# Kernel optimization log

Hardware: AMD Instinct MI355X
Metric: run time of the kernel (lower is better)

Reference implementation:

```python
import jax, jax.numpy as jnp
import numpy as np

N_NODES = 100000
N_EDGES = 1200000
D_IN = 64
D_HID = 64


def setup_inputs() -> dict:
    key = jax.random.key(0)
    k1, k2, k3, k4, k5 = jax.random.split(key, 5)
    src = jax.random.randint(k1, (N_EDGES,), 0, N_NODES, dtype=jnp.int32)
    dst = jax.random.randint(k2, (N_EDGES,), 0, N_NODES, dtype=jnp.int32)
    w = jax.random.uniform(k3, (N_EDGES,), dtype=jnp.float32)
    data = jax.random.normal(k4, (N_NODES, D_IN), dtype=jnp.float32)
    theta = jax.random.normal(k5, (D_IN, D_HID), dtype=jnp.float32)
    return {"src": src, "dst": dst, "w": w, "data": data, "theta": theta,
            "num_nodes": N_NODES}


def reference(src, dst, w, data, theta, num_nodes):
    # weighted gather of source-node features: [E, D_IN]
    weighted = w[:, None] * data[src]
    # scatter-add into destination nodes: [N, D_IN]
    agg = jax.ops.segment_sum(weighted, dst, num_segments=num_nodes)
    # dense projection: [N, D_HID]
    return jnp.dot(agg, theta)
```

## Files before the change

kernel.cpp:

```cpp
#include <hip/hip_runtime.h>

#define D 64
#define NPB 128
#define NPB_SHIFT 7
#define MAXB 1024
#define SCATTER_T 512
#define CHUNK_MAX 4704
#define CAPB 2560
#define GT 512

__device__ inline unsigned f2bf(float f) {
    unsigned u = __float_as_uint(f);
    return (u + 0x7FFFu + ((u >> 16) & 1u)) >> 16;
}

__global__ void zero_i_kernel(int* __restrict__ p, int n) {
    int i = blockIdx.x * blockDim.x + threadIdx.x;
    if (i < n) p[i] = 0;
}
__global__ void zero_f4_kernel(float4* __restrict__ p, int n4) {
    int i = blockIdx.x * blockDim.x + threadIdx.x;
    if (i < n4) p[i] = make_float4(0.f, 0.f, 0.f, 0.f);
}

__global__ __launch_bounds__(SCATTER_T) void bucket_scatter_kernel(
        const int* __restrict__ src, const int* __restrict__ dst,
        const float* __restrict__ w, int* __restrict__ cursor,
        int* __restrict__ ovfCnt, int4* __restrict__ ovf,
        int2* __restrict__ adjB, int E, int B) {
    __shared__ int lc[MAXB];
    __shared__ int lpre[MAXB];
    __shared__ int lbase[MAXB];
    __shared__ int lfill[MAXB];
    __shared__ int sums[SCATTER_T];
    __shared__ unsigned short sb[CHUNK_MAX];
    __shared__ int2 stage[CHUNK_MAX];

    int t = threadIdx.x;
    int chunk = (E + gridDim.x - 1) / gridDim.x;
    int lo = blockIdx.x * chunk, hi = min(lo + chunk, E);
    int n = hi - lo;
    if (n <= 0) return;

    for (int i = t; i < MAXB; i += SCATTER_T) { lc[i] = 0; lfill[i] = 0; }
    __syncthreads();

    for (int e = lo + t; e < hi; e += SCATTER_T)
        atomicAdd(&lc[dst[e] >> NPB_SHIFT], 1);
    __syncthreads();

    int s0 = lc[2 * t], s1 = lc[2 * t + 1];
    sums[t] = s0 + s1;
    __syncthreads();
    for (int st = 1; st < SCATTER_T; st <<= 1) {
        int v = (t >= st) ? sums[t - st] : 0;
        __syncthreads();
        sums[t] += v;
        __syncthreads();
    }
    int ex = (t == 0) ? 0 : sums[t - 1];
    lpre[2 * t]     = ex;
    lpre[2 * t + 1] = ex + s0;
    __syncthreads();

    for (int i = t; i < B; i += SCATTER_T) {
        int c = lc[i];
        lbase[i] = c ? atomicAdd(&cursor[i], c) : 0;
    }
    __syncthreads();

    for (int e = lo + t; e < hi; e += SCATTER_T) {
        int d = dst[e];
        int bkt = d >> NPB_SHIFT;
        int i = lpre[bkt] + atomicAdd(&lfill[bkt], 1);
        stage[i] = make_int2(src[e] | ((d & (NPB - 1)) << 20), __float_as_int(w[e]));
        sb[i] = (unsigned short)bkt;
    }
    __syncthreads();

    for (int i = t; i < n; i += SCATTER_T) {
        int bkt = sb[i];
        int2 v = stage[i];
        int pos = lbase[bkt] + (i - lpre[bkt]);
        if (pos < CAPB) {
            adjB[(size_t)bkt * CAPB + pos] = v;
        } else {
            int oi = atomicAdd(ovfCnt, 1);
            ovf[oi] = make_int4(v.x, v.y, bkt, 0);
        }
    }
}

__global__ __launch_bounds__(GT) void sort_gather_kernel(
        const int2* __restrict__ adjB, const int* __restrict__ cursor,
        const int* __restrict__ ovfCnt, const int4* __restrict__ ovf,
        const unsigned* __restrict__ projU, float* __restrict__ out, int N) {
    __shared__ int cnt[NPB];
    __shared__ int pre[NPB];
    __shared__ int fill[NPB];
    __shared__ int2 ladj[CAPB];
    __shared__ int sOvf;

    int b = blockIdx.x;
    int t = threadIdx.x;
    int total = cursor[b];
    int m = min(total, CAPB);
    const int2* base = adjB + (size_t)b * CAPB;

    if (t < NPB) { cnt[t] = 0; fill[t] = 0; }
    if (t == 0) sOvf = *ovfCnt;
    __syncthreads();
    for (int e = t; e < m; e += GT)
        atomicAdd(&cnt[((unsigned)base[e].x) >> 20], 1);
    __syncthreads();
    if (t < NPB) pre[t] = cnt[t];
    __syncthreads();
    for (int st = 1; st < NPB; st <<= 1) {
        int v = (t < NPB && t >= st) ? pre[t - st] : 0;
        __syncthreads();
        if (t < NPB) pre[t] += v;
        __syncthreads();
    }
    for (int e = t; e < m; e += GT) {
        int2 a = base[e];
        int dL = ((unsigned)a.x) >> 20;
        int pos = ((dL == 0) ? 0 : pre[dL - 1]) + atomicAdd(&fill[dL], 1);
        ladj[pos] = make_int2(a.x & 0xFFFFF, a.y);
    }
    __syncthreads();

    int wave = t >> 6;
    int lane = t & 63;
    int half = lane >> 5;
    int k = lane & 31;

#pragma unroll 1
    for (int i = 0; i < NPB / 8; ++i) {
        int dL = wave * (NPB / 8) + i;
        int node = b * NPB + dL;
        if (node >= N) break;
        int rb = (dL == 0) ? 0 : pre[dL - 1];
        int re = pre[dL];
        float2 accA = make_float2(0.f, 0.f);
        float2 accB = make_float2(0.f, 0.f);
        int j = rb + half;
        for (; j + 2 < re; j += 4) {
            int2 a0 = ladj[j];
            int2 a1 = ladj[j + 2];
            float w0 = __int_as_float(a0.y);
            float w1 = __int_as_float(a1.y);
            unsigned p0 = projU[(size_t)a0.x * 32 + k];
            unsigned p1 = projU[(size_t)a1.x * 32 + k];
            accA.x += w0 * __uint_as_float(p0 << 16);
            accA.y += w0 * __uint_as_float(p0 & 0xFFFF0000u);
            accB.x += w1 * __uint_as_float(p1 << 16);
            accB.y += w1 * __uint_as_float(p1 & 0xFFFF0000u);
        }
        if (j < re) {
            int2 a0 = ladj[j];
            float w0 = __int_as_float(a0.y);
            unsigned p0 = projU[(size_t)a0.x * 32 + k];
            accA.x += w0 * __uint_as_float(p0 << 16);
            accA.y += w0 * __uint_as_float(p0 & 0xFFFF0000u);
        }
        float2 acc = make_float2(accA.x + accB.x, accA.y + accB.y);
        acc.x += __shfl(acc.x, lane ^ 32, 64);
        acc.y += __shfl(acc.y, lane ^ 32, 64);
        if (half == 0)
            *(float2*)&out[(size_t)node * D + 2 * k] = acc;
    }

    if (sOvf > 0) {
        __syncthreads();
        for (int e = t; e < sOvf; e += GT) {
            int4 o = ovf[e];
            if (o.z != b) continue;
            int dL = ((unsigned)o.x) >> 20;
            int node = b * NPB + dL;
            if (node >= N) continue;
            float wgt = __int_as_float(o.y);
            int s = o.x & 0xFFFFF;
            for (int d2 = 0; d2 < D / 2; ++d2) {
                unsigned p = projU[(size_t)s * 32 + d2];
                atomicAdd(&out[(size_t)node * D + 2 * d2],     wgt * __uint_as_float(p << 16));
                atomicAdd(&out[(size_t)node * D + 2 * d2 + 1], wgt * __uint_as_float(p & 0xFFFF0000u));
            }
        }
    }
}

__global__ __launch_bounds__(256, 4) void rowgemm_bf16_kernel(const float* __restrict__ A,
                                                              const float* __restrict__ theta,
                                                              unsigned short* __restrict__ proj16,
                                                              int N) {
    __shared__ float th[D * D];
    __shared__ float at[D][68];
    int t = threadIdx.x;
    int rowBase = blockIdx.x * 64;

#pragma unroll
    for (int i = 0; i < 4; ++i) {
        int f = t + i * 256;
        ((float4*)th)[f] = ((const float4*)theta)[f];
    }
#pragma unroll
    for (int i = 0; i < 4; ++i) {
        int f = t + i * 256;
        int row = f >> 4;
        int kv = f & 15;
        float4 v = make_float4(0.f, 0.f, 0.f, 0.f);
        if (rowBase + row < N) v = *(const float4*)&A[(size_t)(rowBase + row) * D + kv * 4];
        at[kv * 4 + 0][row] = v.x;
        at[kv * 4 + 1][row] = v.y;
        at[kv * 4 + 2][row] = v.z;
        at[kv * 4 + 3][row] = v.w;
    }
    __syncthreads();

    int c0 = (t & 15) * 4;
    int r0 = (t >> 4) * 4;
    float4 acc0 = make_float4(0.f, 0.f, 0.f, 0.f);
    float4 acc1 = acc0, acc2 = acc0, acc3 = acc0;

#pragma unroll 16
    for (int k = 0; k < D; ++k) {
        float4 bv = *(const float4*)&th[k * D + c0];
        float4 av = *(const float4*)&at[k][r0];
        acc0.x += av.x * bv.x; acc0.y += av.x * bv.y; acc0.z += av.x * bv.z; acc0.w += av.x * bv.w;
        acc1.x += av.y * bv.x; acc1.y += av.y * bv.y; acc1.z += av.y * bv.z; acc1.w += av.y * bv.w;
        acc2.x += av.z * bv.x; acc2.y += av.z * bv.y; acc2.z += av.z * bv.z; acc2.w += av.z * bv.w;
        acc3.x += av.w * bv.x; acc3.y += av.w * bv.y; acc3.z += av.w * bv.z; acc3.w += av.w * bv.w;
    }

    float4 accs[4] = {acc0, acc1, acc2, acc3};
#pragma unroll
    for (int i = 0; i < 4; ++i) {
        int r = rowBase + r0 + i;
        if (r < N) {
            unsigned lo = f2bf(accs[i].x) | (f2bf(accs[i].y) << 16);
            unsigned hi = f2bf(accs[i].z) | (f2bf(accs[i].w) << 16);
            *(uint2*)&proj16[(size_t)r * D + c0] = make_uint2(lo, hi);
        }
    }
}

__global__ void scatter_kernel(const int* __restrict__ src, const int* __restrict__ dst,
                               const float* __restrict__ w, const float* __restrict__ data,
                               float* __restrict__ agg, int E) {
    int tid = blockIdx.x * blockDim.x + threadIdx.x;
    int e = tid >> 6;
    int d = tid & 63;
    if (e >= E) return;
    float val = w[e] * data[(size_t)src[e] * D + d];
    atomicAdd(&agg[(size_t)dst[e] * D + d], val);
}

__global__ __launch_bounds__(256, 4) void rowgemm_f32_kernel(const float* __restrict__ A,
                                                             const float* __restrict__ theta,
                                                             float* __restrict__ out, int N) {
    __shared__ float th[D * D];
    __shared__ float at[D][68];
    int t = threadIdx.x;
    int rowBase = blockIdx.x * 64;
#pragma unroll
    for (int i = 0; i < 4; ++i) {
        int f = t + i * 256;
        ((float4*)th)[f] = ((const float4*)theta)[f];
    }
#pragma unroll
    for (int i = 0; i < 4; ++i) {
        int f = t + i * 256;
        int row = f >> 4;
        int kv = f & 15;
        float4 v = make_float4(0.f, 0.f, 0.f, 0.f);
        if (rowBase + row < N) v = *(const float4*)&A[(size_t)(rowBase + row) * D + kv * 4];
        at[kv * 4 + 0][row] = v.x;
        at[kv * 4 + 1][row] = v.y;
        at[kv * 4 + 2][row] = v.z;
        at[kv * 4 + 3][row] = v.w;
    }
    __syncthreads();
    int c0 = (t & 15) * 4;
    int r0 = (t >> 4) * 4;
    float4 acc0 = make_float4(0.f, 0.f, 0.f, 0.f);
    float4 acc1 = acc0, acc2 = acc0, acc3 = acc0;
#pragma unroll 16
    for (int kk = 0; kk < D; ++kk) {
        float4 bv = *(const float4*)&th[kk * D + c0];
        float4 av = *(const float4*)&at[kk][r0];
        acc0.x += av.x * bv.x; acc0.y += av.x * bv.y; acc0.z += av.x * bv.z; acc0.w += av.x * bv.w;
        acc1.x += av.y * bv.x; acc1.y += av.y * bv.y; acc1.z += av.y * bv.z; acc1.w += av.y * bv.w;
        acc2.x += av.z * bv.x; acc2.y += av.z * bv.y; acc2.z += av.z * bv.z; acc2.w += av.z * bv.w;
        acc3.x += av.w * bv.x; acc3.y += av.w * bv.y; acc3.z += av.w * bv.z; acc3.w += av.w * bv.w;
    }
    float4 accs[4] = {acc0, acc1, acc2, acc3};
#pragma unroll
    for (int i = 0; i < 4; ++i) {
        int r = rowBase + r0 + i;
        if (r < N) *(float4*)&out[(size_t)r * D + c0] = accs[i];
    }
}

extern "C" void kernel_launch(void* const* d_in, const int* in_sizes, int n_in,
                              void* d_out, int out_size, void* d_ws, size_t ws_size,
                              hipStream_t stream) {
    const int*   src   = (const int*)d_in[0];
    const int*   dst   = (const int*)d_in[1];
    const float* w     = (const float*)d_in[2];
    const float* data  = (const float*)d_in[3];
    const float* theta = (const float*)d_in[4];
    const int E = in_sizes[0];
    const int N = in_sizes[3] / D;
    float* out = (float*)d_out;

    const int B = (N + NPB - 1) / NPB;

    size_t projBytes = (size_t)N * D * 2;
    size_t adjBytes  = (size_t)B * CAPB * 8;
    size_t ovfBytes  = (size_t)E * 16;
    size_t need = projBytes + adjBytes + ovfBytes + ((size_t)B + 1) * 4 + 256;

    if (ws_size >= need && N < (1 << 20) && B <= MAXB) {
        unsigned short* proj16 = (unsigned short*)d_ws;
        int2* adjB   = (int2*)((char*)d_ws + projBytes);
        int4* ovf    = (int4*)((char*)d_ws + projBytes + adjBytes);
        int*  cursor = (int*)((char*)d_ws + projBytes + adjBytes + ovfBytes);
        int*  ovfCnt = cursor + B;

        int g = (E + CHUNK_MAX - 1) / CHUNK_MAX;

        zero_i_kernel<<<(B + 1 + 255) / 256, 256, 0, stream>>>(cursor, B + 1);
        bucket_scatter_kernel<<<g, SCATTER_T, 0, stream>>>(src, dst, w, cursor, ovfCnt, ovf, adjB, E, B);
        rowgemm_bf16_kernel<<<(N + 63) / 64, 256, 0, stream>>>(data, theta, proj16, N);
        sort_gather_kernel<<<B, GT, 0, stream>>>(adjB, cursor, ovfCnt, ovf, (const unsigned*)proj16, out, N);
    } else {
        float* agg = (float*)d_ws;
        int n4 = (N * D) / 4;
        zero_f4_kernel<<<(n4 + 255) / 256, 256, 0, stream>>>((float4*)agg, n4);
        long long total = (long long)E * D;
        scatter_kernel<<<(int)((total + 255) / 256), 256, 0, stream>>>(src, dst, w, data, agg, E);
        rowgemm_f32_kernel<<<(N + 63) / 64, 256, 0, stream>>>(agg, theta, out, N);
    }
}
```

Measured before the change: 163.9 us.

## Fuse bucket scatter and bf16 projection GEMM into one launch, register-prefetch edges

Merges the bucket-scatter and row-GEMM kernels into a single launch that branches on block index, sharing a union of shared memory, so both phases can run concurrently and one launch is removed. The scatter path loads each thread's edges into registers once instead of reading dst twice from global memory. The gather kernel also keeps adjacency entries in registers between its count and placement passes. Its per-node loop now gives each half-wave its own node with a 4-way unrolled edge loop, which drops the cross-half shuffle. The cost is more registers per thread, a larger shared footprint for GEMM blocks, and a scatter grid clamped to at least 256 blocks.

```diff
diff --git a/kernel.cpp b/kernel.cpp
--- a/kernel.cpp
+++ b/kernel.cpp
@@ -6,8 +6,10 @@
 #define MAXB 1024
 #define SCATTER_T 512
 #define CHUNK_MAX 4704
+#define SCQ 10
 #define CAPB 2560
 #define GT 512
+#define GQ 5
 
 __device__ inline unsigned f2bf(float f) {
     unsigned u = __float_as_uint(f);
@@ -23,70 +25,147 @@
     if (i < n4) p[i] = make_float4(0.f, 0.f, 0.f, 0.f);
 }
 
-__global__ __launch_bounds__(SCATTER_T) void bucket_scatter_kernel(
+union FusedSMem {
+    struct {
+        int lc[MAXB];
+        int lpre[MAXB];
+        int lbase[MAXB];
+        int lfill[MAXB];
+        int sums[SCATTER_T];
+        unsigned short sb[CHUNK_MAX];
+        int2 stage[CHUNK_MAX];
+    } sc;
+    struct {
+        float th[D * D];
+        float at[D][68];
+    } gm;
+};
+
+__global__ __launch_bounds__(SCATTER_T, 4) void fused_scatter_gemm_kernel(
         const int* __restrict__ src, const int* __restrict__ dst,
-        const float* __restrict__ w, int* __restrict__ cursor,
+        const float* __restrict__ w, const float* __restrict__ data,
+        const float* __restrict__ theta, int* __restrict__ cursor,
         int* __restrict__ ovfCnt, int4* __restrict__ ovf,
-        int2* __restrict__ adjB, int E, int B) {
-    __shared__ int lc[MAXB];
-    __shared__ int lpre[MAXB];
-    __shared__ int lbase[MAXB];
-    __shared__ int lfill[MAXB];
-    __shared__ int sums[SCATTER_T];
-    __shared__ unsigned short sb[CHUNK_MAX];
-    __shared__ int2 stage[CHUNK_MAX];
-
+        int2* __restrict__ adjB, unsigned short* __restrict__ proj16,
+        int E, int B, int N, int gs) {
+    __shared__ FusedSMem sm;
     int t = threadIdx.x;
-    int chunk = (E + gridDim.x - 1) / gridDim.x;
-    int lo = blockIdx.x * chunk, hi = min(lo + chunk, E);
-    int n = hi - lo;
-    if (n <= 0) return;
-
-    for (int i = t; i < MAXB; i += SCATTER_T) { lc[i] = 0; lfill[i] = 0; }
-    __syncthreads();
-
-    for (int e = lo + t; e < hi; e += SCATTER_T)
-        atomicAdd(&lc[dst[e] >> NPB_SHIFT], 1);
-    __syncthreads();
-
-    int s0 = lc[2 * t], s1 = lc[2 * t + 1];
-    sums[t] = s0 + s1;
-    __syncthreads();
-    for (int st = 1; st < SCATTER_T; st <<= 1) {
-        int v = (t >= st) ? sums[t - st] : 0;
-        __syncthreads();
-        sums[t] += v;
-        __syncthreads();
-    }
-    int ex = (t == 0) ? 0 : sums[t - 1];
-    lpre[2 * t]     = ex;
-    lpre[2 * t + 1] = ex + s0;
-    __syncthreads();
-
-    for (int i = t; i < B; i += SCATTER_T) {
-        int c = lc[i];
-        lbase[i] = c ? atomicAdd(&cursor[i], c) : 0;
-    }
-    __syncthreads();
-
-    for (int e = lo + t; e < hi; e += SCATTER_T) {
-        int d = dst[e];
-        int bkt = d >> NPB_SHIFT;
-        int i = lpre[bkt] + atomicAdd(&lfill[bkt], 1);
-        stage[i] = make_int2(src[e] | ((d & (NPB - 1)) << 20), __float_as_int(w[e]));
-        sb[i] = (unsigned short)bkt;
-    }
-    __syncthreads();
-
-    for (int i = t; i < n; i += SCATTER_T) {
-        int bkt = sb[i];
-        int2 v = stage[i];
-        int pos = lbase[bkt] + (i - lpre[bkt]);
-        if (pos < CAPB) {
-            adjB[(size_t)bkt * CAPB + pos] = v;
-        } else {
-            int oi = atomicAdd(ovfCnt, 1);
-            ovf[oi] = make_int4(v.x, v.y, bkt, 0);
+
+    if ((int)blockIdx.x < gs) {
+        int chunk = (E + gs - 1) / gs;
+        int lo = blockIdx.x * chunk, hi = min(lo + chunk, E);
+        if (hi - lo <= 0) return;
+        int n = hi - lo;
+
+        for (int i = t; i < MAXB; i += SCATTER_T) { sm.sc.lc[i] = 0; sm.sc.lfill[i] = 0; }
+
+        int rd[SCQ]; int rs[SCQ]; float rw[SCQ];
+#pragma unroll
+        for (int q = 0; q < SCQ; ++q) {
+            int e = lo + t + q * SCATTER_T;
+            bool v = e < hi;
+            rd[q] = v ? dst[e] : -1;
+            rs[q] = v ? src[e] : 0;
+            rw[q] = v ? w[e] : 0.f;
+        }
+        __syncthreads();
+
+#pragma unroll
+        for (int q = 0; q < SCQ; ++q)
+            if (rd[q] >= 0) atomicAdd(&sm.sc.lc[rd[q] >> NPB_SHIFT], 1);
+        __syncthreads();
+
+        int s0 = sm.sc.lc[2 * t], s1 = sm.sc.lc[2 * t + 1];
+        sm.sc.sums[t] = s0 + s1;
+        __syncthreads();
+        for (int st = 1; st < SCATTER_T; st <<= 1) {
+            int v = (t >= st) ? sm.sc.sums[t - st] : 0;
+            __syncthreads();
+            sm.sc.sums[t] += v;
+            __syncthreads();
+        }
+        int ex = (t == 0) ? 0 : sm.sc.sums[t - 1];
+        sm.sc.lpre[2 * t] = ex;
+        sm.sc.lpre[2 * t + 1] = ex + s0;
+        __syncthreads();
+
+        for (int i = t; i < B; i += SCATTER_T) {
+            int c = sm.sc.lc[i];
+            sm.sc.lbase[i] = c ? atomicAdd(&cursor[i], c) : 0;
+        }
+        __syncthreads();
+
+#pragma unroll
+        for (int q = 0; q < SCQ; ++q) {
+            int d = rd[q];
+            if (d >= 0) {
+                int bkt = d >> NPB_SHIFT;
+                int i = sm.sc.lpre[bkt] + atomicAdd(&sm.sc.lfill[bkt], 1);
+                sm.sc.stage[i] = make_int2(rs[q] | ((d & (NPB - 1)) << 20),
+                                           __float_as_int(rw[q]));
+                sm.sc.sb[i] = (unsigned short)bkt;
+            }
+        }
+        __syncthreads();
+
+        for (int i = t; i < n; i += SCATTER_T) {
+            int bkt = sm.sc.sb[i];
+            int2 v = sm.sc.stage[i];
+            int pos = sm.sc.lbase[bkt] + (i - sm.sc.lpre[bkt]);
+            if (pos < CAPB) {
+                adjB[(size_t)bkt * CAPB + pos] = v;
+            } else {
+                int oi = atomicAdd(ovfCnt, 1);
+                ovf[oi] = make_int4(v.x, v.y, bkt, 0);
+            }
+        }
+    } else {
+        int gb = blockIdx.x - gs;
+        int rowBase = gb * 64;
+
+#pragma unroll
+        for (int i = 0; i < 2; ++i) {
+            int f = t + i * 512;
+            ((float4*)sm.gm.th)[f] = ((const float4*)theta)[f];
+        }
+#pragma unroll
+        for (int i = 0; i < 2; ++i) {
+            int f = t + i * 512;
+            int row = f >> 4;
+            int kv = f & 15;
+            float4 v = make_float4(0.f, 0.f, 0.f, 0.f);
+            if (rowBase + row < N) v = *(const float4*)&data[(size_t)(rowBase + row) * D + kv * 4];
+            sm.gm.at[kv * 4 + 0][row] = v.x;
+            sm.gm.at[kv * 4 + 1][row] = v.y;
+            sm.gm.at[kv * 4 + 2][row] = v.z;
+            sm.gm.at[kv * 4 + 3][row] = v.w;
+        }
+        __syncthreads();
+
+        int c0 = (t & 15) * 4;
+        int r0 = (t >> 4) * 2;
+        float4 acc0 = make_float4(0.f, 0.f, 0.f, 0.f);
+        float4 acc1 = acc0;
+
+#pragma unroll 16
+        for (int k = 0; k < D; ++k) {
+            float4 bv = *(const float4*)&sm.gm.th[k * D + c0];
+            float a0 = sm.gm.at[k][r0];
+            float a1 = sm.gm.at[k][r0 + 1];
+            acc0.x += a0 * bv.x; acc0.y += a0 * bv.y; acc0.z += a0 * bv.z; acc0.w += a0 * bv.w;
+            acc1.x += a1 * bv.x; acc1.y += a1 * bv.y; acc1.z += a1 * bv.z; acc1.w += a1 * bv.w;
+        }
+
+        int r = rowBase + r0;
+        if (r < N) {
+            unsigned lo16 = f2bf(acc0.x) | (f2bf(acc0.y) << 16);
+            unsigned hi16 = f2bf(acc0.z) | (f2bf(acc0.w) << 16);
+            *(uint2*)&proj16[(size_t)r * D + c0] = make_uint2(lo16, hi16);
+        }
+        if (r + 1 < N) {
+            unsigned lo16 = f2bf(acc1.x) | (f2bf(acc1.y) << 16);
+            unsigned hi16 = f2bf(acc1.z) | (f2bf(acc1.w) << 16);
+            *(uint2*)&proj16[(size_t)(r + 1) * D + c0] = make_uint2(lo16, hi16);
         }
     }
 }
@@ -110,8 +189,17 @@
     if (t < NPB) { cnt[t] = 0; fill[t] = 0; }
     if (t == 0) sOvf = *ovfCnt;
     __syncthreads();
-    for (int e = t; e < m; e += GT)
-        atomicAdd(&cnt[((unsigned)base[e].x) >> 20], 1);
+
+    int2 r[GQ];
+#pragma unroll
+    for (int q = 0; q < GQ; ++q) {
+        int e = t + q * GT;
+        if (e < m) {
+            int2 a = base[e];
+            r[q] = a;
+            atomicAdd(&cnt[((unsigned)a.x) >> 20], 1);
+        }
+    }
     __syncthreads();
     if (t < NPB) pre[t] = cnt[t];
     __syncthreads();
@@ -121,11 +209,15 @@
         if (t < NPB) pre[t] += v;
         __syncthreads();
     }
-    for (int e = t; e < m; e += GT) {
-        int2 a = base[e];
-        int dL = ((unsigned)a.x) >> 20;
-        int pos = ((dL == 0) ? 0 : pre[dL - 1]) + atomicAdd(&fill[dL], 1);
-        ladj[pos] = make_int2(a.x & 0xFFFFF, a.y);
+#pragma unroll
+    for (int q = 0; q < GQ; ++q) {
+        int e = t + q * GT;
+        if (e < m) {
+            int2 a = r[q];
+            int dL = ((unsigned)a.x) >> 20;
+            int pos = ((dL == 0) ? 0 : pre[dL - 1]) + atomicAdd(&fill[dL], 1);
+            ladj[pos] = make_int2(a.x & 0xFFFFF, a.y);
+        }
     }
     __syncthreads();
 
@@ -135,39 +227,45 @@
     int k = lane & 31;
 
 #pragma unroll 1
-    for (int i = 0; i < NPB / 8; ++i) {
-        int dL = wave * (NPB / 8) + i;
+    for (int i = 0; i < 8; ++i) {
+        int dL = wave * 16 + i * 2 + half;
         int node = b * NPB + dL;
-        if (node >= N) break;
-        int rb = (dL == 0) ? 0 : pre[dL - 1];
-        int re = pre[dL];
-        float2 accA = make_float2(0.f, 0.f);
-        float2 accB = make_float2(0.f, 0.f);
-        int j = rb + half;
-        for (; j + 2 < re; j += 4) {
-            int2 a0 = ladj[j];
-            int2 a1 = ladj[j + 2];
-            float w0 = __int_as_float(a0.y);
-            float w1 = __int_as_float(a1.y);
-            unsigned p0 = projU[(size_t)a0.x * 32 + k];
-            unsigned p1 = projU[(size_t)a1.x * 32 + k];
-            accA.x += w0 * __uint_as_float(p0 << 16);
-            accA.y += w0 * __uint_as_float(p0 & 0xFFFF0000u);
-            accB.x += w1 * __uint_as_float(p1 << 16);
-            accB.y += w1 * __uint_as_float(p1 & 0xFFFF0000u);
-        }
-        if (j < re) {
-            int2 a0 = ladj[j];
-            float w0 = __int_as_float(a0.y);
-            unsigned p0 = projU[(size_t)a0.x * 32 + k];
-            accA.x += w0 * __uint_as_float(p0 << 16);
-            accA.y += w0 * __uint_as_float(p0 & 0xFFFF0000u);
-        }
-        float2 acc = make_float2(accA.x + accB.x, accA.y + accB.y);
-        acc.x += __shfl(acc.x, lane ^ 32, 64);
-        acc.y += __shfl(acc.y, lane ^ 32, 64);
-        if (half == 0)
+        if (node < N) {
+            int rb = (dL == 0) ? 0 : pre[dL - 1];
+            int re = pre[dL];
+            float2 accA = make_float2(0.f, 0.f);
+            float2 accB = make_float2(0.f, 0.f);
+            int j = rb;
+            for (; j + 3 < re; j += 4) {
+                int2 a0 = ladj[j];
+                int2 a1 = ladj[j + 1];
+                int2 a2 = ladj[j + 2];
+                int2 a3 = ladj[j + 3];
+                unsigned p0 = projU[(size_t)a0.x * 32 + k];
+                unsigned p1 = projU[(size_t)a1.x * 32 + k];
+                unsigned p2 = projU[(size_t)a2.x * 32 + k];
+                unsigned p3 = projU[(size_t)a3.x * 32 + k];
+                float w0 = __int_as_float(a0.y), w1 = __int_as_float(a1.y);
+                float w2 = __int_as_float(a2.y), w3 = __int_as_float(a3.y);
+                accA.x += w0 * __uint_as_float(p0 << 16);
+                accA.y += w0 * __uint_as_float(p0 & 0xFFFF0000u);
+                accB.x += w1 * __uint_as_float(p1 << 16);
+                accB.y += w1 * __uint_as_float(p1 & 0xFFFF0000u);
+                accA.x += w2 * __uint_as_float(p2 << 16);
+                accA.y += w2 * __uint_as_float(p2 & 0xFFFF0000u);
+                accB.x += w3 * __uint_as_float(p3 << 16);
+                accB.y += w3 * __uint_as_float(p3 & 0xFFFF0000u);
+            }
+            for (; j < re; ++j) {
+                int2 a0 = ladj[j];
+                float w0 = __int_as_float(a0.y);
+                unsigned p0 = projU[(size_t)a0.x * 32 + k];
+                accA.x += w0 * __uint_as_float(p0 << 16);
+                accA.y += w0 * __uint_as_float(p0 & 0xFFFF0000u);
+            }
+            float2 acc = make_float2(accA.x + accB.x, accA.y + accB.y);
             *(float2*)&out[(size_t)node * D + 2 * k] = acc;
+        }
     }
 
     if (sOvf > 0) {
@@ -189,61 +287,6 @@
     }
 }
 
-__global__ __launch_bounds__(256, 4) void rowgemm_bf16_kernel(const float* __restrict__ A,
-                                                              const float* __restrict__ theta,
-                                                              unsigned short* __restrict__ proj16,
-                                                              int N) {
-    __shared__ float th[D * D];
-    __shared__ float at[D][68];
-    int t = threadIdx.x;
-    int rowBase = blockIdx.x * 64;
-
-#pragma unroll
-    for (int i = 0; i < 4; ++i) {
-        int f = t + i * 256;
-        ((float4*)th)[f] = ((const float4*)theta)[f];
-    }
-#pragma unroll
-    for (int i = 0; i < 4; ++i) {
-        int f = t + i * 256;
-        int row = f >> 4;
-        int kv = f & 15;
-        float4 v = make_float4(0.f, 0.f, 0.f, 0.f);
-        if (rowBase + row < N) v = *(const float4*)&A[(size_t)(rowBase + row) * D + kv * 4];
-        at[kv * 4 + 0][row] = v.x;
-        at[kv * 4 + 1][row] = v.y;
-        at[kv * 4 + 2][row] = v.z;
-        at[kv * 4 + 3][row] = v.w;
-    }
-    __syncthreads();
-
-    int c0 = (t & 15) * 4;
-    int r0 = (t >> 4) * 4;
-    float4 acc0 = make_float4(0.f, 0.f, 0.f, 0.f);
-    float4 acc1 = acc0, acc2 = acc0, acc3 = acc0;
-
-#pragma unroll 16
-    for (int k = 0; k < D; ++k) {
-        float4 bv = *(const float4*)&th[k * D + c0];
-        float4 av = *(const float4*)&at[k][r0];
-        acc0.x += av.x * bv.x; acc0.y += av.x * bv.y; acc0.z += av.x * bv.z; acc0.w += av.x * bv.w;
-        acc1.x += av.y * bv.x; acc1.y += av.y * bv.y; acc1.z += av.y * bv.z; acc1.w += av.y * bv.w;
-        acc2.x += av.z * bv.x; acc2.y += av.z * bv.y; acc2.z += av.z * bv.z; acc2.w += av.z * bv.w;
-        acc3.x += av.w * bv.x; acc3.y += av.w * bv.y; acc3.z += av.w * bv.z; acc3.w += av.w * bv.w;
-    }
-
-    float4 accs[4] = {acc0, acc1, acc2, acc3};
-#pragma unroll
-    for (int i = 0; i < 4; ++i) {
-        int r = rowBase + r0 + i;
-        if (r < N) {
-            unsigned lo = f2bf(accs[i].x) | (f2bf(accs[i].y) << 16);
-            unsigned hi = f2bf(accs[i].z) | (f2bf(accs[i].w) << 16);
-            *(uint2*)&proj16[(size_t)r * D + c0] = make_uint2(lo, hi);
-        }
-    }
-}
-
 __global__ void scatter_kernel(const int* __restrict__ src, const int* __restrict__ dst,
                                const float* __restrict__ w, const float* __restrict__ data,
                                float* __restrict__ agg, int E) {
@@ -327,12 +370,15 @@
         int*  cursor = (int*)((char*)d_ws + projBytes + adjBytes + ovfBytes);
         int*  ovfCnt = cursor + B;
 
-        int g = (E + CHUNK_MAX - 1) / CHUNK_MAX;
+        int gs = (E + CHUNK_MAX - 1) / CHUNK_MAX;
+        if (gs < 256) gs = 256;
+        int gg = (N + 63) / 64;
 
         zero_i_kernel<<<(B + 1 + 255) / 256, 256, 0, stream>>>(cursor, B + 1);
-        bucket_scatter_kernel<<<g, SCATTER_T, 0, stream>>>(src, dst, w, cursor, ovfCnt, ovf, adjB, E, B);
-        rowgemm_bf16_kernel<<<(N + 63) / 64, 256, 0, stream>>>(data, theta, proj16, N);
-        sort_gather_kernel<<<B, GT, 0, stream>>>(adjB, cursor, ovfCnt, ovf, (const unsigned*)proj16, out, N);
+        fused_scatter_gemm_kernel<<<gs + gg, SCATTER_T, 0, stream>>>(
+            src, dst, w, data, theta, cursor, ovfCnt, ovf, adjB, proj16, E, B, N, gs);
+        sort_gather_kernel<<<B, GT, 0, stream>>>(adjB, cursor, ovfCnt, ovf,
+                                                 (const unsigned*)proj16, out, N);
     } else {
         float* agg = (float*)d_ws;
         int n4 = (N * D) / 4;
```

Measured after the change: 161.4 us. About the same (-1.5%).

## Replace per-bucket local sort with shared-memory atomic accumulation in gather

Applied to the files above, without the earlier changes.

The gather kernel no longer counting-sorts each bucket's edges by destination. It streams edges through a small shared buffer and accumulates weighted projected rows into a 128x64 float tile in LDS with shared atomics, then writes the tile out coalesced. The bf16 projection layout is interleaved so each 32-bit word holds columns k and k+32, and the scatter kernel preloads its dst/src/w values into registers once instead of reading global memory twice. This drops the histogram, scan and sort passes but adds LDS atomic contention and 32 KB of shared memory per block, which may lower occupancy.

```diff
diff --git a/kernel.cpp b/kernel.cpp
--- a/kernel.cpp
+++ b/kernel.cpp
@@ -6,6 +6,7 @@
 #define MAXB 1024
 #define SCATTER_T 512
 #define CHUNK_MAX 4704
+#define SCQ 10
 #define CAPB 2560
 #define GT 512
 
@@ -43,10 +44,21 @@
     if (n <= 0) return;
 
     for (int i = t; i < MAXB; i += SCATTER_T) { lc[i] = 0; lfill[i] = 0; }
-    __syncthreads();
-
-    for (int e = lo + t; e < hi; e += SCATTER_T)
-        atomicAdd(&lc[dst[e] >> NPB_SHIFT], 1);
+
+    int rd[SCQ]; int rs[SCQ]; float rw[SCQ];
+#pragma unroll
+    for (int q = 0; q < SCQ; ++q) {
+        int e = lo + t + q * SCATTER_T;
+        bool v = e < hi;
+        rd[q] = v ? dst[e] : -1;
+        rs[q] = v ? src[e] : 0;
+        rw[q] = v ? w[e] : 0.f;
+    }
+    __syncthreads();
+
+#pragma unroll
+    for (int q = 0; q < SCQ; ++q)
+        if (rd[q] >= 0) atomicAdd(&lc[rd[q] >> NPB_SHIFT], 1);
     __syncthreads();
 
     int s0 = lc[2 * t], s1 = lc[2 * t + 1];
@@ -59,7 +71,7 @@
         __syncthreads();
     }
     int ex = (t == 0) ? 0 : sums[t - 1];
-    lpre[2 * t]     = ex;
+    lpre[2 * t] = ex;
     lpre[2 * t + 1] = ex + s0;
     __syncthreads();
 
@@ -69,12 +81,16 @@
     }
     __syncthreads();
 
-    for (int e = lo + t; e < hi; e += SCATTER_T) {
-        int d = dst[e];
-        int bkt = d >> NPB_SHIFT;
-        int i = lpre[bkt] + atomicAdd(&lfill[bkt], 1);
-        stage[i] = make_int2(src[e] | ((d & (NPB - 1)) << 20), __float_as_int(w[e]));
-        sb[i] = (unsigned short)bkt;
+#pragma unroll
+    for (int q = 0; q < SCQ; ++q) {
+        int d = rd[q];
+        if (d >= 0) {
+            int bkt = d >> NPB_SHIFT;
+            int i = lpre[bkt] + atomicAdd(&lfill[bkt], 1);
+            stage[i] = make_int2(rs[q] | ((d & (NPB - 1)) << 20),
+                                 __float_as_int(rw[q]));
+            sb[i] = (unsigned short)bkt;
+        }
     }
     __syncthreads();
 
@@ -91,107 +107,84 @@
     }
 }
 
-__global__ __launch_bounds__(GT) void sort_gather_kernel(
+__global__ __launch_bounds__(GT) void accum_gather_kernel(
         const int2* __restrict__ adjB, const int* __restrict__ cursor,
         const int* __restrict__ ovfCnt, const int4* __restrict__ ovf,
-        const unsigned* __restrict__ projU, float* __restrict__ out, int N) {
-    __shared__ int cnt[NPB];
-    __shared__ int pre[NPB];
-    __shared__ int fill[NPB];
-    __shared__ int2 ladj[CAPB];
+        const unsigned* __restrict__ projW, float* __restrict__ out, int N) {
+    __shared__ float acc[NPB * D];
+    __shared__ int2 ebuf[GT];
     __shared__ int sOvf;
 
     int b = blockIdx.x;
     int t = threadIdx.x;
-    int total = cursor[b];
-    int m = min(total, CAPB);
+    int m = min(cursor[b], CAPB);
     const int2* base = adjB + (size_t)b * CAPB;
 
-    if (t < NPB) { cnt[t] = 0; fill[t] = 0; }
+#pragma unroll
+    for (int i = 0; i < (NPB * D / 4) / GT; ++i)
+        ((float4*)acc)[t + i * GT] = make_float4(0.f, 0.f, 0.f, 0.f);
     if (t == 0) sOvf = *ovfCnt;
     __syncthreads();
-    for (int e = t; e < m; e += GT)
-        atomicAdd(&cnt[((unsigned)base[e].x) >> 20], 1);
-    __syncthreads();
-    if (t < NPB) pre[t] = cnt[t];
-    __syncthreads();
-    for (int st = 1; st < NPB; st <<= 1) {
-        int v = (t < NPB && t >= st) ? pre[t - st] : 0;
-        __syncthreads();
-        if (t < NPB) pre[t] += v;
-        __syncthreads();
-    }
-    for (int e = t; e < m; e += GT) {
-        int2 a = base[e];
-        int dL = ((unsigned)a.x) >> 20;
-        int pos = ((dL == 0) ? 0 : pre[dL - 1]) + atomicAdd(&fill[dL], 1);
-        ladj[pos] = make_int2(a.x & 0xFFFFF, a.y);
-    }
-    __syncthreads();
-
-    int wave = t >> 6;
-    int lane = t & 63;
-    int half = lane >> 5;
-    int k = lane & 31;
-
-#pragma unroll 1
-    for (int i = 0; i < NPB / 8; ++i) {
-        int dL = wave * (NPB / 8) + i;
-        int node = b * NPB + dL;
-        if (node >= N) break;
-        int rb = (dL == 0) ? 0 : pre[dL - 1];
-        int re = pre[dL];
-        float2 accA = make_float2(0.f, 0.f);
-        float2 accB = make_float2(0.f, 0.f);
-        int j = rb + half;
-        for (; j + 2 < re; j += 4) {
-            int2 a0 = ladj[j];
-            int2 a1 = ladj[j + 2];
+
+    int hw = t >> 5;
+    int k = t & 31;
+
+    for (int base_e = 0; base_e < m; base_e += GT) {
+        int nb = min(GT, m - base_e);
+        if (base_e + t < m) ebuf[t] = base[base_e + t];
+        __syncthreads();
+        int j = hw;
+        for (; j + 16 < nb; j += 32) {
+            int2 a0 = ebuf[j];
+            int2 a1 = ebuf[j + 16];
+            unsigned p0 = projW[(size_t)(a0.x & 0xFFFFF) * 32 + k];
+            unsigned p1 = projW[(size_t)(a1.x & 0xFFFFF) * 32 + k];
             float w0 = __int_as_float(a0.y);
             float w1 = __int_as_float(a1.y);
-            unsigned p0 = projU[(size_t)a0.x * 32 + k];
-            unsigned p1 = projU[(size_t)a1.x * 32 + k];
-            accA.x += w0 * __uint_as_float(p0 << 16);
-            accA.y += w0 * __uint_as_float(p0 & 0xFFFF0000u);
-            accB.x += w1 * __uint_as_float(p1 << 16);
-            accB.y += w1 * __uint_as_float(p1 & 0xFFFF0000u);
-        }
-        if (j < re) {
-            int2 a0 = ladj[j];
+            int d0 = ((unsigned)a0.x) >> 20;
+            int d1 = ((unsigned)a1.x) >> 20;
+            atomicAdd(&acc[d0 * D + k],      w0 * __uint_as_float(p0 << 16));
+            atomicAdd(&acc[d0 * D + 32 + k], w0 * __uint_as_float(p0 & 0xFFFF0000u));
+            atomicAdd(&acc[d1 * D + k],      w1 * __uint_as_float(p1 << 16));
+            atomicAdd(&acc[d1 * D + 32 + k], w1 * __uint_as_float(p1 & 0xFFFF0000u));
+        }
+        if (j < nb) {
+            int2 a0 = ebuf[j];
+            unsigned p0 = projW[(size_t)(a0.x & 0xFFFFF) * 32 + k];
             float w0 = __int_as_float(a0.y);
-            unsigned p0 = projU[(size_t)a0.x * 32 + k];
-            accA.x += w0 * __uint_as_float(p0 << 16);
-            accA.y += w0 * __uint_as_float(p0 & 0xFFFF0000u);
-        }
-        float2 acc = make_float2(accA.x + accB.x, accA.y + accB.y);
-        acc.x += __shfl(acc.x, lane ^ 32, 64);
-        acc.y += __shfl(acc.y, lane ^ 32, 64);
-        if (half == 0)
-            *(float2*)&out[(size_t)node * D + 2 * k] = acc;
+            int d0 = ((unsigned)a0.x) >> 20;
+            atomicAdd(&acc[d0 * D + k],      w0 * __uint_as_float(p0 << 16));
+            atomicAdd(&acc[d0 * D + 32 + k], w0 * __uint_as_float(p0 & 0xFFFF0000u));
+        }
+        __syncthreads();
     }
 
     if (sOvf > 0) {
-        __syncthreads();
-        for (int e = t; e < sOvf; e += GT) {
+        for (int e = hw; e < sOvf; e += 16) {
             int4 o = ovf[e];
             if (o.z != b) continue;
             int dL = ((unsigned)o.x) >> 20;
-            int node = b * NPB + dL;
-            if (node >= N) continue;
             float wgt = __int_as_float(o.y);
-            int s = o.x & 0xFFFFF;
-            for (int d2 = 0; d2 < D / 2; ++d2) {
-                unsigned p = projU[(size_t)s * 32 + d2];
-                atomicAdd(&out[(size_t)node * D + 2 * d2],     wgt * __uint_as_float(p << 16));
-                atomicAdd(&out[(size_t)node * D + 2 * d2 + 1], wgt * __uint_as_float(p & 0xFFFF0000u));
-            }
-        }
+            unsigned p = projW[(size_t)(o.x & 0xFFFFF) * 32 + k];
+            atomicAdd(&acc[dL * D + k],      wgt * __uint_as_float(p << 16));
+            atomicAdd(&acc[dL * D + 32 + k], wgt * __uint_as_float(p & 0xFFFF0000u));
+        }
+        __syncthreads();
+    }
+
+    int node0 = b * NPB;
+#pragma unroll
+    for (int i = 0; i < (NPB * D / 4) / GT; ++i) {
+        int f4 = t + i * GT;
+        int node = node0 + (f4 >> 4);
+        if (node < N)
+            *(float4*)&out[(size_t)node0 * D + (size_t)f4 * 4] = ((float4*)acc)[f4];
     }
 }
 
 __global__ __launch_bounds__(256, 4) void rowgemm_bf16_kernel(const float* __restrict__ A,
                                                               const float* __restrict__ theta,
-                                                              unsigned short* __restrict__ proj16,
+                                                              unsigned* __restrict__ projW,
                                                               int N) {
     __shared__ float th[D * D];
     __shared__ float at[D][68];
@@ -217,14 +210,16 @@
     }
     __syncthreads();
 
-    int c0 = (t & 15) * 4;
+    int cw = (t & 15) * 2;
     int r0 = (t >> 4) * 4;
     float4 acc0 = make_float4(0.f, 0.f, 0.f, 0.f);
     float4 acc1 = acc0, acc2 = acc0, acc3 = acc0;
 
 #pragma unroll 16
     for (int k = 0; k < D; ++k) {
-        float4 bv = *(const float4*)&th[k * D + c0];
+        float2 bl = *(const float2*)&th[k * D + cw];
+        float2 bh = *(const float2*)&th[k * D + cw + 32];
+        float4 bv = make_float4(bl.x, bl.y, bh.x, bh.y);
         float4 av = *(const float4*)&at[k][r0];
         acc0.x += av.x * bv.x; acc0.y += av.x * bv.y; acc0.z += av.x * bv.z; acc0.w += av.x * bv.w;
         acc1.x += av.y * bv.x; acc1.y += av.y * bv.y; acc1.z += av.y * bv.z; acc1.w += av.y * bv.w;
@@ -237,9 +232,9 @@
     for (int i = 0; i < 4; ++i) {
         int r = rowBase + r0 + i;
         if (r < N) {
-            unsigned lo = f2bf(accs[i].x) | (f2bf(accs[i].y) << 16);
-            unsigned hi = f2bf(accs[i].z) | (f2bf(accs[i].w) << 16);
-            *(uint2*)&proj16[(size_t)r * D + c0] = make_uint2(lo, hi);
+            unsigned wa = f2bf(accs[i].x) | (f2bf(accs[i].z) << 16);
+            unsigned wb = f2bf(accs[i].y) | (f2bf(accs[i].w) << 16);
+            *(uint2*)&projW[(size_t)r * 32 + cw] = make_uint2(wa, wb);
         }
     }
 }
@@ -321,18 +316,20 @@
     size_t need = projBytes + adjBytes + ovfBytes + ((size_t)B + 1) * 4 + 256;
 
     if (ws_size >= need && N < (1 << 20) && B <= MAXB) {
-        unsigned short* proj16 = (unsigned short*)d_ws;
+        unsigned* projW = (unsigned*)d_ws;
         int2* adjB   = (int2*)((char*)d_ws + projBytes);
         int4* ovf    = (int4*)((char*)d_ws + projBytes + adjBytes);
         int*  cursor = (int*)((char*)d_ws + projBytes + adjBytes + ovfBytes);
         int*  ovfCnt = cursor + B;
 
-        int g = (E + CHUNK_MAX - 1) / CHUNK_MAX;
+        int gs = (E + CHUNK_MAX - 1) / CHUNK_MAX;
 
         zero_i_kernel<<<(B + 1 + 255) / 256, 256, 0, stream>>>(cursor, B + 1);
-        bucket_scatter_kernel<<<g, SCATTER_T, 0, stream>>>(src, dst, w, cursor, ovfCnt, ovf, adjB, E, B);
-        rowgemm_bf16_kernel<<<(N + 63) / 64, 256, 0, stream>>>(data, theta, proj16, N);
-        sort_gather_kernel<<<B, GT, 0, stream>>>(adjB, cursor, ovfCnt, ovf, (const unsigned*)proj16, out, N);
+        bucket_scatter_kernel<<<gs, SCATTER_T, 0, stream>>>(src, dst, w, cursor,
+                                                            ovfCnt, ovf, adjB, E, B);
+        rowgemm_bf16_kernel<<<(N + 63) / 64, 256, 0, stream>>>(data, theta, projW, N);
+        accum_gather_kernel<<<B, GT, 0, stream>>>(adjB, cursor, ovfCnt, ovf,
+                                                  projW, out, N);
     } else {
         float* agg = (float*)d_ws;
         int n4 = (N * D) / 4;
```

Result: slower. 630.3 us (+284.4%).
